# Kernel tuning notes

Measured on AMD Instinct MI355X. Metric: run time of the kernel, lower is better.

## Reference

```python
import jax, jax.numpy as jnp
import numpy as np

B, C, HEADS, DH = 2, 1280, 20, 64
INNER = HEADS * DH
HW = 64
S = HW * HW
L = 77
ENC = 4096
GROUPS = 32
EPS = 1e-5
CREG = 1.0     # creg_ in __init__
NOATTN = 1.0   # global noattn
NORES = 1.0    # global noresidual


def setup_inputs() -> dict:
    key = jax.random.key(0)
    ks = jax.random.split(key, 10)
    std = 0.02
    return {
        "x": jax.random.normal(ks[0], (B, C, HW, HW), jnp.float32),
        "text": jax.random.normal(ks[1], (B, L, ENC), jnp.float32),
        "gn_gamma": jnp.ones((C,), jnp.float32),
        "gn_beta": jnp.zeros((C,), jnp.float32),
        "ln_gamma": jnp.ones((ENC,), jnp.float32),
        "ln_beta": jnp.zeros((ENC,), jnp.float32),
        "Wq": jax.random.normal(ks[2], (C, INNER), jnp.float32) * std,
        "bq": jnp.zeros((INNER,), jnp.float32),
        "Wk": jax.random.normal(ks[3], (ENC, INNER), jnp.float32) * std,
        "bk": jnp.zeros((INNER,), jnp.float32),
        "Wv": jax.random.normal(ks[4], (ENC, INNER), jnp.float32) * std,
        "bv": jnp.zeros((INNER,), jnp.float32),
        "Wo": jax.random.normal(ks[5], (INNER, C), jnp.float32) * std,
        "bo": jnp.zeros((C,), jnp.float32),
        "size_reg": jax.random.uniform(ks[6], (1, S, L), jnp.float32),
        "treg": jax.random.uniform(ks[7], (1,), jnp.float32),
        "mask": jax.random.randint(ks[8], (1, S, L), 0, 2, jnp.int32),
    }


def _group_norm(h, gamma, beta):
    # h: [B, C, S]; GroupNorm over (C//GROUPS, S) per group
    hg = h.reshape(B, GROUPS, -1)
    mu = hg.mean(-1, keepdims=True)
    var = hg.var(-1, keepdims=True)
    hn = ((hg - mu) * jax.lax.rsqrt(var + EPS)).reshape(B, C, S)
    return hn * gamma[None, :, None] + beta[None, :, None]


def _layer_norm(t, gamma, beta):
    mu = t.mean(-1, keepdims=True)
    var = t.var(-1, keepdims=True)
    return (t - mu) * jax.lax.rsqrt(var + EPS) * gamma + beta


def reference(x, text, gn_gamma, gn_beta, ln_gamma, ln_beta, Wq, bq, Wk, bk,
              Wv, bv, Wo, bo, size_reg, treg, mask):
    residual = x                              # [B, C, HW, HW]
    h = x.reshape(B, C, S)                    # spatial tokens
    h = _group_norm(h, gn_gamma, gn_beta).transpose(0, 2, 1)   # [B, S, C]
    enc = _layer_norm(text, ln_gamma, ln_beta)                  # [B, L, ENC]

    # head_to_batch_dim (out_dim=3): [B, T, inner] -> [B*heads, T, dh]
    q = (h @ Wq + bq).reshape(B, S, HEADS, DH).transpose(0, 2, 1, 3).reshape(B * HEADS, S, DH)
    k = (enc @ Wk + bk).reshape(B, L, HEADS, DH).transpose(0, 2, 1, 3).reshape(B * HEADS, L, DH)
    v = (enc @ Wv + bv).reshape(B, L, HEADS, DH).transpose(0, 2, 1, 3).reshape(B * HEADS, L, DH)

    scale = DH ** -0.5
    sim = jnp.einsum('bsd,bld->bsl', q, k) * scale            # [B*H, S, L]

    # region regularization applied only to the conditional (second) half
    half = (B * HEADS) // 2
    sim_u, sim_c = sim[:half], sim[half:]
    mn = sim_c.min(-1, keepdims=True)
    mx = sim_c.max(-1, keepdims=True)
    m = mask > 0                                               # [1, S, L] broadcasts over heads
    w = size_reg * CREG * treg[0]
    sim_c = sim_c + jnp.where(m, w, 0.0) * (mx - sim_c) - jnp.where(m, 0.0, w) * (sim_c - mn)
    sim = jnp.concatenate([sim_u, sim_c], axis=0)

    probs = jax.nn.softmax(sim, axis=-1)
    out = jnp.einsum('bsl,bld->bsd', probs, v)                 # [B*H, S, DH]
    # batch_to_head_dim: [B*H, S, DH] -> [B, S, inner]
    out = out.reshape(B, HEADS, S, DH).transpose(0, 2, 1, 3).reshape(B, S, INNER)
    out = out @ Wo + bo                                        # to_out[0]; dropout p=0
    out = out.transpose(0, 2, 1).reshape(residual.shape)       # [B, C, HW, HW]
    return out * NOATTN + residual * NORES
```

## Files before the change

### kernel.cpp

```cpp
#include <hip/hip_runtime.h>

typedef __bf16 bf16_t;
typedef __bf16 bf16x8 __attribute__((ext_vector_type(8)));
typedef float  f32x4  __attribute__((ext_vector_type(4)));
typedef unsigned int u32x4 __attribute__((ext_vector_type(4)));


__global__ __launch_bounds__(256) void k_prep(
    const float* __restrict__ x, const float* __restrict__ text,
    const float* __restrict__ lng, const float* __restrict__ lnb,
    const float* __restrict__ w0, const float* __restrict__ w1,
    const float* __restrict__ w2, const float* __restrict__ w3,
    bf16_t* __restrict__ o0, bf16_t* __restrict__ o1,
    bf16_t* __restrict__ o2, bf16_t* __restrict__ o3,
    float* __restrict__ partial, bf16_t* __restrict__ enc)
{
  __shared__ float smemf[64 * 33];
  const int bid = blockIdx.x;
  const int t   = threadIdx.x;

  if (bid < 6720) {
    int z, lb;
    if      (bid < 800)  { z = 0; lb = bid; }
    else if (bid < 1600) { z = 1; lb = bid - 800; }
    else if (bid < 4160) { z = 2; lb = bid - 1600; }
    else                 { z = 3; lb = bid - 4160; }
    const float* in  = (z == 0) ? w0 : (z == 1) ? w1 : (z == 2) ? w2 : w3;
    bf16_t*      out = (z == 0) ? o0 : (z == 1) ? o1 : (z == 2) ? o2 : o3;
    const int R  = (z < 2) ? 1280 : 4096;
    const int c0 = (lb % 40) * 32;
    const int r0 = (lb / 40) * 64;
    float (*tile)[33] = (float(*)[33])smemf;
#pragma unroll
    for (int it = 0; it < 8; ++it) {
      int r = it * 8 + (t >> 5), c = t & 31;
      tile[r][c] = in[(size_t)(r0 + r) * 1280 + c0 + c];
    }
    __syncthreads();
    const int oc  = t >> 3;
    const int seg = t & 7;
    bf16x8 o;
#pragma unroll
    for (int e = 0; e < 8; ++e) o[e] = (bf16_t)tile[seg * 8 + e][oc];
    *(bf16x8*)(out + (size_t)(c0 + oc) * R + r0 + seg * 8) = o;
  } else if (bid < 8768) {
    const int pb    = bid - 6720;
    const int bg    = pb >> 5;
    const int chunk = pb & 31;
    const float* p  = x + (size_t)bg * 163840 + (size_t)chunk * 5120;
    float s1 = 0.f, s2 = 0.f;
#pragma unroll
    for (int it = 0; it < 5; ++it) {
      float4 v = *(const float4*)(p + (size_t)(it * 256 + t) * 4);
      s1 += v.x + v.y + v.z + v.w;
      s2 += v.x * v.x + v.y * v.y + v.z * v.z + v.w * v.w;
    }
#pragma unroll
    for (int off = 32; off > 0; off >>= 1) {
      s1 += __shfl_down(s1, off);
      s2 += __shfl_down(s2, off);
    }
    float* r1 = smemf;
    float* r2 = smemf + 4;
    if ((t & 63) == 0) { r1[t >> 6] = s1; r2[t >> 6] = s2; }
    __syncthreads();
    if (t == 0) {
      partial[pb * 2]     = r1[0] + r1[1] + r1[2] + r1[3];
      partial[pb * 2 + 1] = r2[0] + r2[1] + r2[2] + r2[3];
    }
  } else {
    const int row = bid - 8768;
    const float* p = text + (size_t)row * 4096;
    float s1 = 0.f, s2 = 0.f;
    for (int i = t; i < 1024; i += 256) {
      float4 v = *(const float4*)(p + (size_t)i * 4);
      s1 += v.x + v.y + v.z + v.w;
      s2 += v.x * v.x + v.y * v.y + v.z * v.z + v.w * v.w;
    }
#pragma unroll
    for (int off = 32; off > 0; off >>= 1) {
      s1 += __shfl_down(s1, off);
      s2 += __shfl_down(s2, off);
    }
    float* r1 = smemf;
    float* r2 = smemf + 4;
    float* sh = smemf + 8;
    if ((t & 63) == 0) { r1[t >> 6] = s1; r2[t >> 6] = s2; }
    __syncthreads();
    if (t == 0) {
      float t1 = r1[0] + r1[1] + r1[2] + r1[3];
      float t2 = r2[0] + r2[1] + r2[2] + r2[3];
      const float invN = 1.0f / 4096.0f;
      float mu  = t1 * invN;
      float var = t2 * invN - mu * mu;
      sh[0] = mu;
      sh[1] = rsqrtf(var + 1e-5f);
    }
    __syncthreads();
    const float mu = sh[0], rs = sh[1];
    for (int i = t; i < 1024; i += 256) {
      float4 v  = *(const float4*)(p + (size_t)i * 4);
      float4 gg = *(const float4*)(lng + (size_t)i * 4);
      float4 bb = *(const float4*)(lnb + (size_t)i * 4);
      bf16_t* o = enc + (size_t)row * 4096 + (size_t)i * 4;
      o[0] = (bf16_t)((v.x - mu) * rs * gg.x + bb.x);
      o[1] = (bf16_t)((v.y - mu) * rs * gg.y + bb.y);
      o[2] = (bf16_t)((v.z - mu) * rs * gg.z + bb.z);
      o[3] = (bf16_t)((v.w - mu) * rs * gg.w + bb.w);
    }
  }
}

__global__ __launch_bounds__(256) void k_gn_apply(
    const float* __restrict__ x, const float* __restrict__ partial,
    const float* __restrict__ gamma, const float* __restrict__ beta,
    bf16_t* __restrict__ h)
{
  __shared__ float tile[64][65];
  __shared__ float sst[64];
  const int s0 = blockIdx.x * 64;
  const int c0 = blockIdx.y * 64;
  const int b  = blockIdx.z;
  const int t  = threadIdx.x;

  {
    const int g = t >> 3, j = t & 7;
    const int base = ((b * 32 + g) * 32) * 2;
    float s1 = 0.f, s2 = 0.f;
#pragma unroll
    for (int k = 0; k < 4; ++k) {
      s1 += partial[base + (j + 8 * k) * 2];
      s2 += partial[base + (j + 8 * k) * 2 + 1];
    }
    s1 += __shfl_down(s1, 1); s2 += __shfl_down(s2, 1);
    s1 += __shfl_down(s1, 2); s2 += __shfl_down(s2, 2);
    s1 += __shfl_down(s1, 4); s2 += __shfl_down(s2, 4);
    if (j == 0) {
      const float invN = 1.0f / 163840.0f;
      float mu  = s1 * invN;
      float var = s2 * invN - mu * mu;
      sst[g * 2]     = mu;
      sst[g * 2 + 1] = rsqrtf(var + 1e-5f);
    }
  }
#pragma unroll
  for (int it = 0; it < 16; ++it) {
    int cl = it * 4 + (t >> 6);
    int sl = t & 63;
    tile[cl][sl] = x[((size_t)(b * 1280 + c0 + cl) << 12) + s0 + sl];
  }
  __syncthreads();
#pragma unroll
  for (int it = 0; it < 2; ++it) {
    int i  = it * 256 + t;
    int sl = i >> 3;
    int cg = i & 7;
    bf16x8 o;
#pragma unroll
    for (int e = 0; e < 8; ++e) {
      int c  = c0 + cg * 8 + e;
      int g  = c / 40;
      float mu = sst[g * 2];
      float rs = sst[g * 2 + 1];
      o[e] = (bf16_t)((tile[cg * 8 + e][sl] - mu) * rs * gamma[c] + beta[c]);
    }
    *(bf16x8*)(h + (size_t)(b * 4096 + s0 + sl) * 1280 + c0 + cg * 8) = o;
  }
}

template <int EPI>
__global__ __launch_bounds__(256, 3) void k_gemm(
    const bf16_t* __restrict__ A, const bf16_t* __restrict__ BT,
    const float* __restrict__ bias, bf16_t* __restrict__ outb,
    float* __restrict__ outf, const float* __restrict__ xres,
    float* __restrict__ dout, int M, int lda, int klen, int nnt, int nst)
{
  __shared__ alignas(16) bf16_t smem[24576];
  const int tid  = threadIdx.x;
  const int lane = tid & 63;
  const int wv   = tid >> 6;
  const int wm   = wv >> 1, wn = wv & 1;

  const int cpx  = gridDim.x >> 3;
  const int nbid = (blockIdx.x & 7) * cpx + (blockIdx.x >> 3);
  const int mt   = nbid / nnt, ntile = nbid % nnt;
  const int m0   = mt * 128;
  const int n0   = ntile * 64;
  const int kbeg = blockIdx.z * klen;

  f32x4 acc[4][2];
  const f32x4 fz = {0.f, 0.f, 0.f, 0.f};
#pragma unroll
  for (int i = 0; i < 4; ++i)
#pragma unroll
    for (int j = 0; j < 2; ++j) acc[i][j] = fz;

  auto stage = [&](int buf, int kt) {
    bf16_t* sA = smem + buf * 8192;
    bf16_t* sB = smem + 16384 + buf * 4096;
#pragma unroll
    for (int it = 0; it < 4; ++it) {
      int slot = it * 256 + tid;
      int row  = slot >> 3, ch = slot & 7;
      int grow = m0 + row; if (grow > M - 1) grow = M - 1;
      const bf16_t* ga = A + (size_t)grow * lda + kt + ((ch ^ (row & 7)) << 3);
      __builtin_amdgcn_global_load_lds(
          (const __attribute__((address_space(1))) void*)ga,
          (__attribute__((address_space(3))) void*)((char*)sA + slot * 16),
          16, 0, 0);
    }
#pragma unroll
    for (int it = 0; it < 2; ++it) {
      int slot = it * 256 + tid;
      int row  = slot >> 3, ch = slot & 7;
      const bf16_t* gb = BT + (size_t)(n0 + row) * lda + kt + ((ch ^ (row & 7)) << 3);
      __builtin_amdgcn_global_load_lds(
          (const __attribute__((address_space(1))) void*)gb,
          (__attribute__((address_space(3))) void*)((char*)sB + slot * 16),
          16, 0, 0);
    }
  };

  const int nt_k = klen >> 6;
  stage(0, kbeg);
  if (nt_k > 1) stage(1, kbeg + 64);

  for (int t = 0; t < nt_k; ++t) {
    if (t + 1 < nt_k) { asm volatile("s_waitcnt vmcnt(6)" ::: "memory"); }
    else              { asm volatile("s_waitcnt vmcnt(0)" ::: "memory"); }
    __builtin_amdgcn_s_barrier();
    const char* pA = (const char*)(smem + (t & 1) * 8192);
    const char* pB = (const char*)(smem + 16384 + (t & 1) * 4096);
#pragma unroll
    for (int ks = 0; ks < 2; ++ks) {
      const int kb = ks * 64 + ((lane >> 4) << 4);
      bf16x8 af[4], bfg[2];
#pragma unroll
      for (int i = 0; i < 4; ++i) {
        int r = wm * 64 + i * 16 + (lane & 15);
        af[i] = *(const bf16x8*)(pA + r * 128 + (kb ^ ((r & 7) << 4)));
      }
#pragma unroll
      for (int j = 0; j < 2; ++j) {
        int c = wn * 32 + j * 16 + (lane & 15);
        bfg[j] = *(const bf16x8*)(pB + c * 128 + (kb ^ ((c & 7) << 4)));
      }
#pragma unroll
      for (int i = 0; i < 4; ++i)
#pragma unroll
        for (int j = 0; j < 2; ++j)
          acc[i][j] = __builtin_amdgcn_mfma_f32_16x16x32_bf16(af[i], bfg[j], acc[i][j], 0, 0, 0);
    }
    asm volatile("s_waitcnt lgkmcnt(0)" ::: "memory");
    __builtin_amdgcn_s_barrier();
    if (t + 2 < nt_k) stage(t & 1, kbeg + (t + 2) * 64);
  }

  if (EPI == 0) {
    bf16_t* cst = smem;
#pragma unroll
    for (int j = 0; j < 2; ++j) {
      const int n  = n0 + wn * 32 + j * 16 + (lane & 15);
      const float bs = bias[n];
      const int cl = wn * 32 + j * 16 + (lane & 15);
#pragma unroll
      for (int i = 0; i < 4; ++i) {
        const int rl = wm * 64 + i * 16 + ((lane >> 4) << 2);
#pragma unroll
        for (int r = 0; r < 4; ++r)
          cst[(rl + r) * 76 + cl] = (bf16_t)(acc[i][j][r] + bs);
      }
    }
    __syncthreads();
#pragma unroll
    for (int it = 0; it < 4; ++it) {
      int slot = it * 256 + tid;
      int row = slot >> 3, ch = slot & 7;
      u32x4 d = *(const u32x4*)(cst + row * 76 + ch * 8);
      *(u32x4*)(outb + (size_t)(m0 + row) * 1280 + n0 + ch * 8) = d;
    }
  } else {
#pragma unroll
    for (int i = 0; i < 4; ++i) {
      const int mrow = m0 + wm * 64 + i * 16 + ((lane >> 4) << 2);
#pragma unroll
      for (int j = 0; j < 2; ++j) {
        const int n = n0 + wn * 32 + j * 16 + (lane & 15);
        if (EPI == 2) {
          const int b = mrow >> 12, s = mrow & 4095;
          const size_t off = ((size_t)(b * 1280 + n) << 12) + s;
          const float bs = bias[n];
          const float4 xr = *(const float4*)(xres + off);
          float4 o;
          o.x = acc[i][j][0] + bs + xr.x;
          o.y = acc[i][j][1] + bs + xr.y;
          o.z = acc[i][j][2] + bs + xr.z;
          o.w = acc[i][j][3] + bs + xr.w;
          *(float4*)(dout + off) = o;
        } else {
#pragma unroll
          for (int r = 0; r < 4; ++r)
            if (mrow + r < M)
              outf[(size_t)blockIdx.z * 154 * nst + (size_t)(mrow + r) * nst + n] = acc[i][j][r];
        }
      }
    }
  }
}

__global__ __launch_bounds__(256) void k_kv_reduce(
    const float* __restrict__ part, const float* __restrict__ bk,
    const float* __restrict__ bv, bf16_t* __restrict__ kb, bf16_t* __restrict__ vb)
{
  const int i4 = (blockIdx.x * 256 + threadIdx.x) * 4;
  if (i4 >= 154 * 2560) return;
  const int r = i4 / 2560, n = i4 % 2560;
  float4 s = (n < 1280) ? *(const float4*)(bk + n) : *(const float4*)(bv + n - 1280);
#pragma unroll
  for (int sp = 0; sp < 8; ++sp) {
    float4 p = *(const float4*)(part + (size_t)sp * (154 * 2560) + i4);
    s.x += p.x; s.y += p.y; s.z += p.z; s.w += p.w;
  }
  bf16_t* dst = (n < 1280) ? (kb + (size_t)r * 1280 + n) : (vb + (size_t)r * 1280 + n - 1280);
  dst[0] = (bf16_t)s.x; dst[1] = (bf16_t)s.y; dst[2] = (bf16_t)s.z; dst[3] = (bf16_t)s.w;
}

__global__ __launch_bounds__(256) void k_attn(
    const bf16_t* __restrict__ q, const bf16_t* __restrict__ kbuf,
    const bf16_t* __restrict__ vbuf, bf16_t* __restrict__ ao,
    const float* __restrict__ size_reg, const int* __restrict__ mask,
    const float* __restrict__ treg)
{
  __shared__ alignas(16) bf16_t sQ[64 * 64];
  __shared__ alignas(16) bf16_t sK[80 * 64];
  __shared__ alignas(16) bf16_t sVT[64 * 104];
  __shared__ alignas(16) bf16_t sP[4 * 16 * 104];
  const int s0   = blockIdx.x * 64;
  const int bh   = blockIdx.y;
  const int b    = bh / 20, head = bh % 20;
  const int tid  = threadIdx.x, lane = tid & 63, wv = tid >> 6;
  const int ntok = lane & 15;

  const u32x4 uz = {0u, 0u, 0u, 0u};
  for (int i = tid; i < 832; i += 256) ((u32x4*)sVT)[i] = uz;
  for (int i = tid; i < 832; i += 256) ((u32x4*)sP)[i]  = uz;

  const size_t qbase = ((size_t)(b * 4096 + s0)) * 1280 + head * 64;
  for (int slot = tid; slot < 512; slot += 256) {
    int row = slot >> 3, ch = slot & 7;
    u32x4 d = *(const u32x4*)(q + qbase + (size_t)row * 1280 + ((ch ^ (row & 7)) << 3));
    *(u32x4*)((char*)sQ + slot * 16) = d;
  }
  const size_t kvbase = ((size_t)(b * 77)) * 1280 + head * 64;
  for (int slot = tid; slot < 640; slot += 256) {
    int tok = slot >> 3, ch = slot & 7;
    u32x4 d = uz;
    if (tok < 77)
      d = *(const u32x4*)(kbuf + kvbase + (size_t)tok * 1280 + ((ch ^ (tok & 7)) << 3));
    *(u32x4*)((char*)sK + slot * 16) = d;
  }
  __syncthreads();
  for (int e = tid; e < 77 * 64; e += 256) {
    int tok = e >> 6, dh = e & 63;
    sVT[dh * 104 + tok] = vbuf[kvbase + (size_t)tok * 1280 + dh];
  }
  __syncthreads();

  f32x4 sim[5];
  const f32x4 fz = {0.f, 0.f, 0.f, 0.f};
#pragma unroll
  for (int nf = 0; nf < 5; ++nf) sim[nf] = fz;
  const int qrow = wv * 16 + (lane & 15);
#pragma unroll
  for (int ks = 0; ks < 2; ++ks) {
    const int kb = ks * 64 + ((lane >> 4) << 4);
    bf16x8 aq = *(const bf16x8*)((const char*)sQ + qrow * 128 + (kb ^ ((qrow & 7) << 4)));
#pragma unroll
    for (int nf = 0; nf < 5; ++nf) {
      int tok = nf * 16 + ntok;
      bf16x8 bk = *(const bf16x8*)((const char*)sK + tok * 128 + (kb ^ ((tok & 7) << 4)));
      sim[nf] = __builtin_amdgcn_mfma_f32_16x16x32_bf16(aq, bk, sim[nf], 0, 0, 0);
    }
  }

  float vv[5][4];
#pragma unroll
  for (int nf = 0; nf < 5; ++nf)
#pragma unroll
    for (int r = 0; r < 4; ++r) vv[nf][r] = sim[nf][r] * 0.125f;

  const int rbase = s0 + wv * 16 + ((lane >> 4) << 2);

  if (b == 1) {
    const float tr = treg[0];
#pragma unroll
    for (int r = 0; r < 4; ++r) {
      float mx = -1e30f, mn = 1e30f;
#pragma unroll
      for (int nf = 0; nf < 5; ++nf)
        if (nf * 16 + ntok < 77) { mx = fmaxf(mx, vv[nf][r]); mn = fminf(mn, vv[nf][r]); }
#pragma unroll
      for (int m = 1; m < 16; m <<= 1) {
        mx = fmaxf(mx, __shfl_xor(mx, m));
        mn = fminf(mn, __shfl_xor(mn, m));
      }
      const int srow = rbase + r;
#pragma unroll
      for (int nf = 0; nf < 5; ++nf) {
        int l = nf * 16 + ntok;
        if (l < 77) {
          float w  = size_reg[srow * 77 + l] * tr;
          int   mk = mask[srow * 77 + l];
          float v  = vv[nf][r];
          vv[nf][r] = (mk > 0) ? v + w * (mx - v) : v - w * (v - mn);
        }
      }
    }
  }

#pragma unroll
  for (int r = 0; r < 4; ++r) {
    float mx = -1e30f;
#pragma unroll
    for (int nf = 0; nf < 5; ++nf)
      if (nf * 16 + ntok < 77) mx = fmaxf(mx, vv[nf][r]);
#pragma unroll
    for (int m = 1; m < 16; m <<= 1) mx = fmaxf(mx, __shfl_xor(mx, m));
    float p[5]; float sm = 0.f;
#pragma unroll
    for (int nf = 0; nf < 5; ++nf) {
      bool val = (nf * 16 + ntok) < 77;
      p[nf] = val ? __expf(vv[nf][r] - mx) : 0.f;
      sm += p[nf];
    }
#pragma unroll
    for (int m = 1; m < 16; m <<= 1) sm += __shfl_xor(sm, m);
    const float inv = 1.0f / sm;
    const int prow = ((lane >> 4) << 2) + r;
#pragma unroll
    for (int nf = 0; nf < 5; ++nf)
      sP[wv * 1664 + prow * 104 + nf * 16 + ntok] = (bf16_t)(p[nf] * inv);
  }
  __syncthreads();

  f32x4 o[4];
#pragma unroll
  for (int fd = 0; fd < 4; ++fd) o[fd] = fz;
#pragma unroll
  for (int ks = 0; ks < 3; ++ks) {
    const int kb = ks * 64 + ((lane >> 4) << 4);
    bf16x8 ap = *(const bf16x8*)((const char*)sP + wv * 3328 + (lane & 15) * 208 + kb);
#pragma unroll
    for (int fd = 0; fd < 4; ++fd) {
      bf16x8 bv = *(const bf16x8*)((const char*)sVT + (fd * 16 + (lane & 15)) * 208 + kb);
      o[fd] = __builtin_amdgcn_mfma_f32_16x16x32_bf16(ap, bv, o[fd], 0, 0, 0);
    }
  }
  const size_t obase =
      ((size_t)(b * 4096 + s0 + wv * 16 + ((lane >> 4) << 2))) * 1280 + head * 64;
#pragma unroll
  for (int fd = 0; fd < 4; ++fd)
#pragma unroll
    for (int r = 0; r < 4; ++r)
      ao[obase + (size_t)r * 1280 + fd * 16 + (lane & 15)] = (bf16_t)o[fd][r];
}

extern "C" void kernel_launch(void* const* d_in, const int* in_sizes, int n_in,
                              void* d_out, int out_size, void* d_ws, size_t ws_size,
                              hipStream_t stream)
{
  const float* x    = (const float*)d_in[0];
  const float* text = (const float*)d_in[1];
  const float* gng  = (const float*)d_in[2];
  const float* gnb  = (const float*)d_in[3];
  const float* lng  = (const float*)d_in[4];
  const float* lnb  = (const float*)d_in[5];
  const float* Wq   = (const float*)d_in[6];
  const float* bq   = (const float*)d_in[7];
  const float* Wk   = (const float*)d_in[8];
  const float* bk   = (const float*)d_in[9];
  const float* Wv   = (const float*)d_in[10];
  const float* bv   = (const float*)d_in[11];
  const float* Wo   = (const float*)d_in[12];
  const float* bo   = (const float*)d_in[13];
  const float* sreg = (const float*)d_in[14];
  const float* treg = (const float*)d_in[15];
  const int*   msk  = (const int*)d_in[16];
  float* out = (float*)d_out;

  char* ws = (char*)d_ws;
  size_t off = 0;
  auto alloc = [&](size_t bytes) {
    char* p = ws + off;
    off += (bytes + 255) & ~(size_t)255;
    return p;
  };
  float*  partial = (float*)alloc(2048 * 2 * sizeof(float));
  bf16_t* WqT = (bf16_t*)alloc((size_t)1280 * 1280 * 2);
  bf16_t* WkT = (bf16_t*)alloc((size_t)1280 * 4096 * 2);
  bf16_t* WvT = (bf16_t*)alloc((size_t)1280 * 4096 * 2);
  bf16_t* WoT = (bf16_t*)alloc((size_t)1280 * 1280 * 2);
  bf16_t* h   = (bf16_t*)alloc((size_t)8192 * 1280 * 2);
  bf16_t* enc = (bf16_t*)alloc((size_t)154 * 4096 * 2);
  bf16_t* qb  = (bf16_t*)alloc((size_t)8192 * 1280 * 2);
  bf16_t* kb  = (bf16_t*)alloc((size_t)154 * 1280 * 2);
  bf16_t* vb  = (bf16_t*)alloc((size_t)154 * 1280 * 2);
  float*  part = (float*)alloc((size_t)8 * 154 * 2560 * sizeof(float));

  k_prep<<<8922, 256, 0, stream>>>(x, text, lng, lnb, Wq, Wo, Wk, Wv,
                                   WqT, WoT, WkT, WvT, partial, enc);

  k_gn_apply<<<dim3(64, 20, 2), 256, 0, stream>>>(x, partial, gng, gnb, h);

  k_gemm<0><<<dim3(1280), 256, 0, stream>>>(h, WqT, bq, qb, nullptr, nullptr, nullptr,
                                            8192, 1280, 1280, 20, 1280);
  k_gemm<1><<<dim3(80, 1, 8), 256, 0, stream>>>(enc, WkT, nullptr, nullptr, part, nullptr, nullptr,
                                                154, 4096, 512, 40, 2560);
  k_kv_reduce<<<385, 256, 0, stream>>>(part, bk, bv, kb, vb);

  k_attn<<<dim3(64, 40), 256, 0, stream>>>(qb, kb, vb, h, sreg, msk, treg);

  k_gemm<2><<<dim3(1280), 256, 0, stream>>>(h, WoT, bo, nullptr, nullptr, x, out,
                                            8192, 1280, 1280, 20, 1280);
}
```

Before: 165.4 us.

## Use 256x256 GEMM tiles and merge GN-apply, KV GEMM and reduce launches

The Q and output projections now use a new 512-thread GEMM kernel with 256x256 tiles and a double-buffered LDS pipeline. Staging is issued early in each k-step, and s_setprio is raised around the MFMA section. The group-norm apply and the split-K KV projection GEMM are merged into one heterogeneous launch, and the KV reduction is folded into the Q-GEMM launch as extra blocks. This cuts launch count and raises data reuse per tile, but 160 blocks of 512 threads may leave CUs underused. The bigger LDS and register footprint also limits occupancy to one block.

```diff
diff --git a/kernel.cpp b/kernel.cpp
--- a/kernel.cpp
+++ b/kernel.cpp
@@ -111,82 +111,81 @@
   }
 }
 
-__global__ __launch_bounds__(256) void k_gn_apply(
+__global__ __launch_bounds__(256, 3) void k_gnapply_kv(
     const float* __restrict__ x, const float* __restrict__ partial,
     const float* __restrict__ gamma, const float* __restrict__ beta,
-    bf16_t* __restrict__ h)
+    bf16_t* __restrict__ h,
+    const bf16_t* __restrict__ enc, const bf16_t* __restrict__ WkT,
+    float* __restrict__ part)
 {
-  __shared__ float tile[64][65];
-  __shared__ float sst[64];
-  const int s0 = blockIdx.x * 64;
-  const int c0 = blockIdx.y * 64;
-  const int b  = blockIdx.z;
-  const int t  = threadIdx.x;
-
-  {
-    const int g = t >> 3, j = t & 7;
-    const int base = ((b * 32 + g) * 32) * 2;
-    float s1 = 0.f, s2 = 0.f;
-#pragma unroll
-    for (int k = 0; k < 4; ++k) {
-      s1 += partial[base + (j + 8 * k) * 2];
-      s2 += partial[base + (j + 8 * k) * 2 + 1];
-    }
-    s1 += __shfl_down(s1, 1); s2 += __shfl_down(s2, 1);
-    s1 += __shfl_down(s1, 2); s2 += __shfl_down(s2, 2);
-    s1 += __shfl_down(s1, 4); s2 += __shfl_down(s2, 4);
-    if (j == 0) {
-      const float invN = 1.0f / 163840.0f;
-      float mu  = s1 * invN;
-      float var = s2 * invN - mu * mu;
-      sst[g * 2]     = mu;
-      sst[g * 2 + 1] = rsqrtf(var + 1e-5f);
-    }
-  }
-#pragma unroll
-  for (int it = 0; it < 16; ++it) {
-    int cl = it * 4 + (t >> 6);
-    int sl = t & 63;
-    tile[cl][sl] = x[((size_t)(b * 1280 + c0 + cl) << 12) + s0 + sl];
-  }
-  __syncthreads();
-#pragma unroll
-  for (int it = 0; it < 2; ++it) {
-    int i  = it * 256 + t;
-    int sl = i >> 3;
-    int cg = i & 7;
-    bf16x8 o;
-#pragma unroll
-    for (int e = 0; e < 8; ++e) {
-      int c  = c0 + cg * 8 + e;
-      int g  = c / 40;
-      float mu = sst[g * 2];
-      float rs = sst[g * 2 + 1];
-      o[e] = (bf16_t)((tile[cg * 8 + e][sl] - mu) * rs * gamma[c] + beta[c]);
-    }
-    *(bf16x8*)(h + (size_t)(b * 4096 + s0 + sl) * 1280 + c0 + cg * 8) = o;
-  }
-}
-
-template <int EPI>
-__global__ __launch_bounds__(256, 3) void k_gemm(
-    const bf16_t* __restrict__ A, const bf16_t* __restrict__ BT,
-    const float* __restrict__ bias, bf16_t* __restrict__ outb,
-    float* __restrict__ outf, const float* __restrict__ xres,
-    float* __restrict__ dout, int M, int lda, int klen, int nnt, int nst)
-{
-  __shared__ alignas(16) bf16_t smem[24576];
-  const int tid  = threadIdx.x;
+  __shared__ alignas(16) char smraw[49152];
+  const int bid = blockIdx.x;
+  const int tid = threadIdx.x;
+
+  if (bid < 2560) {
+    float (*tile)[65] = (float(*)[65])smraw;
+    float* sst = (float*)(smraw + 64 * 65 * sizeof(float));
+    const int s0 = (bid & 63) * 64;
+    const int c0 = ((bid >> 6) % 20) * 64;
+    const int b  = bid / 1280;
+    {
+      const int g = tid >> 3, j = tid & 7;
+      const int base = ((b * 32 + g) * 32) * 2;
+      float s1 = 0.f, s2 = 0.f;
+#pragma unroll
+      for (int k = 0; k < 4; ++k) {
+        s1 += partial[base + (j + 8 * k) * 2];
+        s2 += partial[base + (j + 8 * k) * 2 + 1];
+      }
+      s1 += __shfl_down(s1, 1); s2 += __shfl_down(s2, 1);
+      s1 += __shfl_down(s1, 2); s2 += __shfl_down(s2, 2);
+      s1 += __shfl_down(s1, 4); s2 += __shfl_down(s2, 4);
+      if (j == 0) {
+        const float invN = 1.0f / 163840.0f;
+        float mu  = s1 * invN;
+        float var = s2 * invN - mu * mu;
+        sst[g * 2]     = mu;
+        sst[g * 2 + 1] = rsqrtf(var + 1e-5f);
+      }
+    }
+#pragma unroll
+    for (int it = 0; it < 16; ++it) {
+      int cl = it * 4 + (tid >> 6);
+      int sl = tid & 63;
+      tile[cl][sl] = x[((size_t)(b * 1280 + c0 + cl) << 12) + s0 + sl];
+    }
+    __syncthreads();
+#pragma unroll
+    for (int it = 0; it < 2; ++it) {
+      int i  = it * 256 + tid;
+      int sl = i >> 3;
+      int cg = i & 7;
+      bf16x8 o;
+#pragma unroll
+      for (int e = 0; e < 8; ++e) {
+        int c  = c0 + cg * 8 + e;
+        int g  = c / 40;
+        float mu = sst[g * 2];
+        float rs = sst[g * 2 + 1];
+        o[e] = (bf16_t)((tile[cg * 8 + e][sl] - mu) * rs * gamma[c] + beta[c]);
+      }
+      *(bf16x8*)(h + (size_t)(b * 4096 + s0 + sl) * 1280 + c0 + cg * 8) = o;
+    }
+    return;
+  }
+
+  bf16_t* smem = (bf16_t*)smraw;
   const int lane = tid & 63;
   const int wv   = tid >> 6;
   const int wm   = wv >> 1, wn = wv & 1;
-
-  const int cpx  = gridDim.x >> 3;
-  const int nbid = (blockIdx.x & 7) * cpx + (blockIdx.x >> 3);
-  const int mt   = nbid / nnt, ntile = nbid % nnt;
-  const int m0   = mt * 128;
-  const int n0   = ntile * 64;
-  const int kbeg = blockIdx.z * klen;
+  const int xx   = bid - 2560;
+  const int sk   = xx / 80;
+  const int tl   = xx % 80;
+  const int nb   = (tl & 7) * 10 + (tl >> 3);
+  const int m0   = (nb / 40) * 128;
+  const int n0   = (nb % 40) * 64;
+  const int kbeg = sk * 512;
+  const int lda  = 4096;
 
   f32x4 acc[4][2];
   const f32x4 fz = {0.f, 0.f, 0.f, 0.f};
@@ -202,8 +201,8 @@
     for (int it = 0; it < 4; ++it) {
       int slot = it * 256 + tid;
       int row  = slot >> 3, ch = slot & 7;
-      int grow = m0 + row; if (grow > M - 1) grow = M - 1;
-      const bf16_t* ga = A + (size_t)grow * lda + kt + ((ch ^ (row & 7)) << 3);
+      int grow = m0 + row; if (grow > 153) grow = 153;
+      const bf16_t* ga = enc + (size_t)grow * lda + kt + ((ch ^ (row & 7)) << 3);
       __builtin_amdgcn_global_load_lds(
           (const __attribute__((address_space(1))) void*)ga,
           (__attribute__((address_space(3))) void*)((char*)sA + slot * 16),
@@ -213,6 +212,125 @@
     for (int it = 0; it < 2; ++it) {
       int slot = it * 256 + tid;
       int row  = slot >> 3, ch = slot & 7;
+      const bf16_t* gb = WkT + (size_t)(n0 + row) * lda + kt + ((ch ^ (row & 7)) << 3);
+      __builtin_amdgcn_global_load_lds(
+          (const __attribute__((address_space(1))) void*)gb,
+          (__attribute__((address_space(3))) void*)((char*)sB + slot * 16),
+          16, 0, 0);
+    }
+  };
+
+  stage(0, kbeg);
+  stage(1, kbeg + 64);
+
+  for (int t = 0; t < 8; ++t) {
+    if (t + 1 < 8) { asm volatile("s_waitcnt vmcnt(6)" ::: "memory"); }
+    else           { asm volatile("s_waitcnt vmcnt(0)" ::: "memory"); }
+    __builtin_amdgcn_s_barrier();
+    const char* pA = (const char*)(smem + (t & 1) * 8192);
+    const char* pB = (const char*)(smem + 16384 + (t & 1) * 4096);
+#pragma unroll
+    for (int ks = 0; ks < 2; ++ks) {
+      const int kb = ks * 64 + ((lane >> 4) << 4);
+      bf16x8 af[4], bfg[2];
+#pragma unroll
+      for (int i = 0; i < 4; ++i) {
+        int r = wm * 64 + i * 16 + (lane & 15);
+        af[i] = *(const bf16x8*)(pA + r * 128 + (kb ^ ((r & 7) << 4)));
+      }
+#pragma unroll
+      for (int j = 0; j < 2; ++j) {
+        int c = wn * 32 + j * 16 + (lane & 15);
+        bfg[j] = *(const bf16x8*)(pB + c * 128 + (kb ^ ((c & 7) << 4)));
+      }
+#pragma unroll
+      for (int i = 0; i < 4; ++i)
+#pragma unroll
+        for (int j = 0; j < 2; ++j)
+          acc[i][j] = __builtin_amdgcn_mfma_f32_16x16x32_bf16(af[i], bfg[j], acc[i][j], 0, 0, 0);
+    }
+    asm volatile("s_waitcnt lgkmcnt(0)" ::: "memory");
+    __builtin_amdgcn_s_barrier();
+    if (t + 2 < 8) stage(t & 1, kbeg + (t + 2) * 64);
+  }
+
+#pragma unroll
+  for (int i = 0; i < 4; ++i) {
+    const int mrow = m0 + wm * 64 + i * 16 + ((lane >> 4) << 2);
+#pragma unroll
+    for (int j = 0; j < 2; ++j) {
+      const int n = n0 + wn * 32 + j * 16 + (lane & 15);
+#pragma unroll
+      for (int r = 0; r < 4; ++r)
+        if (mrow + r < 154)
+          part[(size_t)sk * (154 * 2560) + (size_t)(mrow + r) * 2560 + n] = acc[i][j][r];
+    }
+  }
+}
+
+template <int EPI>
+__global__ __launch_bounds__(512, 1) void k_gemm256(
+    const bf16_t* __restrict__ A, const bf16_t* __restrict__ BT,
+    const float* __restrict__ bias, bf16_t* __restrict__ outb,
+    const float* __restrict__ xres, float* __restrict__ dout,
+    const float* __restrict__ part, const float* __restrict__ bk,
+    const float* __restrict__ bv, bf16_t* __restrict__ kb, bf16_t* __restrict__ vb)
+{
+  __shared__ alignas(16) bf16_t smem[65536];
+  const int tid = threadIdx.x;
+
+  if (EPI == 0 && blockIdx.x >= 160) {
+    const int i4 = ((blockIdx.x - 160) * 512 + tid) * 4;
+    if (i4 < 154 * 2560) {
+      const int r = i4 / 2560, n = i4 % 2560;
+      float4 s = (n < 1280) ? *(const float4*)(bk + n) : *(const float4*)(bv + n - 1280);
+#pragma unroll
+      for (int sp = 0; sp < 8; ++sp) {
+        float4 p = *(const float4*)(part + (size_t)sp * (154 * 2560) + i4);
+        s.x += p.x; s.y += p.y; s.z += p.z; s.w += p.w;
+      }
+      bf16_t* dst = (n < 1280) ? (kb + (size_t)r * 1280 + n)
+                               : (vb + (size_t)r * 1280 + n - 1280);
+      dst[0] = (bf16_t)s.x; dst[1] = (bf16_t)s.y;
+      dst[2] = (bf16_t)s.z; dst[3] = (bf16_t)s.w;
+    }
+    return;
+  }
+
+  const int lane = tid & 63;
+  const int wv   = tid >> 6;
+  const int wm   = wv >> 2, wn = wv & 3;
+  const int lda  = 1280;
+  const int nt   = 20;
+
+  const int nbid = (blockIdx.x & 7) * 20 + (blockIdx.x >> 3);
+  const int m0   = (nbid / 5) * 256;
+  const int n0   = (nbid % 5) * 256;
+
+  f32x4 acc[8][4];
+  const f32x4 fz = {0.f, 0.f, 0.f, 0.f};
+#pragma unroll
+  for (int i = 0; i < 8; ++i)
+#pragma unroll
+    for (int j = 0; j < 4; ++j) acc[i][j] = fz;
+
+  auto stage_tile = [&](int buf, int kt) {
+    bf16_t* sA = smem + buf * 16384;
+    bf16_t* sB = smem + 32768 + buf * 16384;
+#pragma unroll
+    for (int it = 0; it < 4; ++it) {
+      int slot = it * 512 + tid;
+      int row = slot >> 3, ch = slot & 7;
+      const bf16_t* ga = A + (size_t)(m0 + row) * lda + kt + ((ch ^ (row & 7)) << 3);
+      __builtin_amdgcn_global_load_lds(
+          (const __attribute__((address_space(1))) void*)ga,
+          (__attribute__((address_space(3))) void*)((char*)sA + slot * 16),
+          16, 0, 0);
+    }
+#pragma unroll
+    for (int it = 0; it < 4; ++it) {
+      int slot = it * 512 + tid;
+      int row = slot >> 3, ch = slot & 7;
       const bf16_t* gb = BT + (size_t)(n0 + row) * lda + kt + ((ch ^ (row & 7)) << 3);
       __builtin_amdgcn_global_load_lds(
           (const __attribute__((address_space(1))) void*)gb,
@@ -221,108 +339,95 @@
     }
   };
 
-  const int nt_k = klen >> 6;
-  stage(0, kbeg);
-  if (nt_k > 1) stage(1, kbeg + 64);
-
-  for (int t = 0; t < nt_k; ++t) {
-    if (t + 1 < nt_k) { asm volatile("s_waitcnt vmcnt(6)" ::: "memory"); }
-    else              { asm volatile("s_waitcnt vmcnt(0)" ::: "memory"); }
+  stage_tile(0, 0);
+
+  for (int t = 0; t < nt; ++t) {
+    asm volatile("s_waitcnt vmcnt(0)" ::: "memory");
     __builtin_amdgcn_s_barrier();
-    const char* pA = (const char*)(smem + (t & 1) * 8192);
-    const char* pB = (const char*)(smem + 16384 + (t & 1) * 4096);
-#pragma unroll
-    for (int ks = 0; ks < 2; ++ks) {
+    const char* pA = (const char*)(smem + (t & 1) * 16384);
+    const char* pB = (const char*)(smem + 32768 + (t & 1) * 16384);
+    bf16x8 bfg[4];
+#pragma unroll
+    for (int p = 0; p < 4; ++p) {
+      const int mg = p & 1, ks = p >> 1;
       const int kb = ks * 64 + ((lane >> 4) << 4);
-      bf16x8 af[4], bfg[2];
+      bf16x8 af[4];
 #pragma unroll
       for (int i = 0; i < 4; ++i) {
-        int r = wm * 64 + i * 16 + (lane & 15);
+        int r = wm * 128 + (mg * 4 + i) * 16 + (lane & 15);
         af[i] = *(const bf16x8*)(pA + r * 128 + (kb ^ ((r & 7) << 4)));
       }
-#pragma unroll
-      for (int j = 0; j < 2; ++j) {
-        int c = wn * 32 + j * 16 + (lane & 15);
-        bfg[j] = *(const bf16x8*)(pB + c * 128 + (kb ^ ((c & 7) << 4)));
-      }
+      if (mg == 0) {
+#pragma unroll
+        for (int j = 0; j < 4; ++j) {
+          int c = wn * 64 + j * 16 + (lane & 15);
+          bfg[j] = *(const bf16x8*)(pB + c * 128 + (kb ^ ((c & 7) << 4)));
+        }
+      }
+      if (p == 0 && t + 1 < nt) stage_tile((t + 1) & 1, (t + 1) * 64);
+      __builtin_amdgcn_s_barrier();
+      __builtin_amdgcn_s_setprio(1);
 #pragma unroll
       for (int i = 0; i < 4; ++i)
 #pragma unroll
-        for (int j = 0; j < 2; ++j)
-          acc[i][j] = __builtin_amdgcn_mfma_f32_16x16x32_bf16(af[i], bfg[j], acc[i][j], 0, 0, 0);
-    }
-    asm volatile("s_waitcnt lgkmcnt(0)" ::: "memory");
-    __builtin_amdgcn_s_barrier();
-    if (t + 2 < nt_k) stage(t & 1, kbeg + (t + 2) * 64);
+        for (int j = 0; j < 4; ++j)
+          acc[mg * 4 + i][j] =
+              __builtin_amdgcn_mfma_f32_16x16x32_bf16(af[i], bfg[j], acc[mg * 4 + i][j], 0, 0, 0);
+      __builtin_amdgcn_s_setprio(0);
+      __builtin_amdgcn_s_barrier();
+    }
   }
 
   if (EPI == 0) {
     bf16_t* cst = smem;
-#pragma unroll
-    for (int j = 0; j < 2; ++j) {
-      const int n  = n0 + wn * 32 + j * 16 + (lane & 15);
-      const float bs = bias[n];
-      const int cl = wn * 32 + j * 16 + (lane & 15);
-#pragma unroll
-      for (int i = 0; i < 4; ++i) {
-        const int rl = wm * 64 + i * 16 + ((lane >> 4) << 2);
-#pragma unroll
-        for (int r = 0; r < 4; ++r)
-          cst[(rl + r) * 76 + cl] = (bf16_t)(acc[i][j][r] + bs);
-      }
-    }
-    __syncthreads();
-#pragma unroll
-    for (int it = 0; it < 4; ++it) {
-      int slot = it * 256 + tid;
-      int row = slot >> 3, ch = slot & 7;
-      u32x4 d = *(const u32x4*)(cst + row * 76 + ch * 8);
-      *(u32x4*)(outb + (size_t)(m0 + row) * 1280 + n0 + ch * 8) = d;
+    float bs[4];
+#pragma unroll
+    for (int j = 0; j < 4; ++j) bs[j] = bias[n0 + wn * 64 + j * 16 + (lane & 15)];
+#pragma unroll
+    for (int mh = 0; mh < 2; ++mh) {
+      __syncthreads();
+      if (wm == mh) {
+#pragma unroll
+        for (int fi = 0; fi < 8; ++fi) {
+          const int rl = fi * 16 + ((lane >> 4) << 2);
+#pragma unroll
+          for (int j = 0; j < 4; ++j) {
+            const int cl = wn * 64 + j * 16 + (lane & 15);
+#pragma unroll
+            for (int r = 0; r < 4; ++r)
+              cst[(rl + r) * 264 + cl] = (bf16_t)(acc[fi][j][r] + bs[j]);
+          }
+        }
+      }
+      __syncthreads();
+#pragma unroll
+      for (int it = 0; it < 8; ++it) {
+        int slot = it * 512 + tid;
+        int row = slot >> 5, ch = slot & 31;
+        u32x4 d = *(const u32x4*)(cst + row * 264 + ch * 8);
+        *(u32x4*)(outb + (size_t)(m0 + mh * 128 + row) * 1280 + n0 + ch * 8) = d;
+      }
     }
   } else {
 #pragma unroll
-    for (int i = 0; i < 4; ++i) {
-      const int mrow = m0 + wm * 64 + i * 16 + ((lane >> 4) << 2);
-#pragma unroll
-      for (int j = 0; j < 2; ++j) {
-        const int n = n0 + wn * 32 + j * 16 + (lane & 15);
-        if (EPI == 2) {
-          const int b = mrow >> 12, s = mrow & 4095;
-          const size_t off = ((size_t)(b * 1280 + n) << 12) + s;
-          const float bs = bias[n];
-          const float4 xr = *(const float4*)(xres + off);
-          float4 o;
-          o.x = acc[i][j][0] + bs + xr.x;
-          o.y = acc[i][j][1] + bs + xr.y;
-          o.z = acc[i][j][2] + bs + xr.z;
-          o.w = acc[i][j][3] + bs + xr.w;
-          *(float4*)(dout + off) = o;
-        } else {
-#pragma unroll
-          for (int r = 0; r < 4; ++r)
-            if (mrow + r < M)
-              outf[(size_t)blockIdx.z * 154 * nst + (size_t)(mrow + r) * nst + n] = acc[i][j][r];
-        }
-      }
-    }
-  }
-}
-
-__global__ __launch_bounds__(256) void k_kv_reduce(
-    const float* __restrict__ part, const float* __restrict__ bk,
-    const float* __restrict__ bv, bf16_t* __restrict__ kb, bf16_t* __restrict__ vb)
-{
-  const int i4 = (blockIdx.x * 256 + threadIdx.x) * 4;
-  if (i4 >= 154 * 2560) return;
-  const int r = i4 / 2560, n = i4 % 2560;
-  float4 s = (n < 1280) ? *(const float4*)(bk + n) : *(const float4*)(bv + n - 1280);
-#pragma unroll
-  for (int sp = 0; sp < 8; ++sp) {
-    float4 p = *(const float4*)(part + (size_t)sp * (154 * 2560) + i4);
-    s.x += p.x; s.y += p.y; s.z += p.z; s.w += p.w;
-  }
-  bf16_t* dst = (n < 1280) ? (kb + (size_t)r * 1280 + n) : (vb + (size_t)r * 1280 + n - 1280);
-  dst[0] = (bf16_t)s.x; dst[1] = (bf16_t)s.y; dst[2] = (bf16_t)s.z; dst[3] = (bf16_t)s.w;
+    for (int fi = 0; fi < 8; ++fi) {
+      const int mrow = m0 + wm * 128 + fi * 16 + ((lane >> 4) << 2);
+      const int b = mrow >> 12, s = mrow & 4095;
+#pragma unroll
+      for (int j = 0; j < 4; ++j) {
+        const int n = n0 + wn * 64 + j * 16 + (lane & 15);
+        const size_t off = ((size_t)(b * 1280 + n) << 12) + s;
+        const float bsv = bias[n];
+        const float4 xr = *(const float4*)(xres + off);
+        float4 o;
+        o.x = acc[fi][j][0] + bsv + xr.x;
+        o.y = acc[fi][j][1] + bsv + xr.y;
+        o.z = acc[fi][j][2] + bsv + xr.z;
+        o.w = acc[fi][j][3] + bsv + xr.w;
+        *(float4*)(dout + off) = o;
+      }
+    }
+  }
 }
 
 __global__ __launch_bounds__(256) void k_attn(
@@ -510,16 +615,13 @@
   k_prep<<<8922, 256, 0, stream>>>(x, text, lng, lnb, Wq, Wo, Wk, Wv,
                                    WqT, WoT, WkT, WvT, partial, enc);
 
-  k_gn_apply<<<dim3(64, 20, 2), 256, 0, stream>>>(x, partial, gng, gnb, h);
-
-  k_gemm<0><<<dim3(1280), 256, 0, stream>>>(h, WqT, bq, qb, nullptr, nullptr, nullptr,
-                                            8192, 1280, 1280, 20, 1280);
-  k_gemm<1><<<dim3(80, 1, 8), 256, 0, stream>>>(enc, WkT, nullptr, nullptr, part, nullptr, nullptr,
-                                                154, 4096, 512, 40, 2560);
-  k_kv_reduce<<<385, 256, 0, stream>>>(part, bk, bv, kb, vb);
+  k_gnapply_kv<<<3200, 256, 0, stream>>>(x, partial, gng, gnb, h, enc, WkT, part);
+
+  k_gemm256<0><<<353, 512, 0, stream>>>(h, WqT, bq, qb, nullptr, nullptr,
+                                        part, bk, bv, kb, vb);
 
   k_attn<<<dim3(64, 40), 256, 0, stream>>>(qb, kb, vb, h, sreg, msk, treg);
 
-  k_gemm<2><<<dim3(1280), 256, 0, stream>>>(h, WoT, bo, nullptr, nullptr, x, out,
-                                            8192, 1280, 1280, 20, 1280);
+  k_gemm256<2><<<160, 512, 0, stream>>>(h, WoT, bo, nullptr, x, out,
+                                        nullptr, nullptr, nullptr, nullptr, nullptr);
 }
```

Result: slower. 180.9 us (+9.4%).
